# Kernel tuning notes

Hardware: AMD Instinct MI355X
Metric: run time of the kernel (lower is better)

Reference implementation:

```python
import jax, jax.numpy as jnp
import numpy as np

D_MODEL = 768
N_HEAD = 12
D_HEAD = 64


def setup_inputs() -> dict:
    key = jax.random.key(0)
    k1, k2, k3, k4, k5 = jax.random.split(key, 5)
    B, T = 8, 1024
    hidden_states = jax.random.normal(k1, (B, T, D_MODEL), dtype=jnp.float32)
    # torch Linear weights are [out, in]; we store [in, out] and use x @ W
    scale_attn = 1.0 / np.sqrt(D_MODEL)
    W_attn = jax.random.normal(k2, (D_MODEL, 3 * D_MODEL), dtype=jnp.float32) * scale_attn
    b_attn = jax.random.normal(k3, (3 * D_MODEL,), dtype=jnp.float32) * 0.02
    W_proj = jax.random.normal(k4, (D_MODEL, D_MODEL), dtype=jnp.float32) * scale_attn
    b_proj = jax.random.normal(k5, (D_MODEL,), dtype=jnp.float32) * 0.02
    return {"hidden_states": hidden_states, "W_attn": W_attn, "b_attn": b_attn,
            "W_proj": W_proj, "b_proj": b_proj}


def reference(hidden_states, W_attn, b_attn, W_proj, b_proj):
    B, T, _ = hidden_states.shape
    qkv = hidden_states @ W_attn + b_attn                     # [B, T, 3*D]
    Q, K, V = jnp.split(qkv, 3, axis=-1)
    def heads(x):  # [B, T, D] -> [B, H, T, d]
        return x.reshape(B, T, N_HEAD, D_HEAD).transpose(0, 2, 1, 3)
    Q, K, V = heads(Q), heads(K), heads(V)
    # past_key_values=None -> T_full == T, q_start == 0: standard causal mask
    scores = jnp.einsum('bhqd,bhkd->bhqk', Q, K) / np.sqrt(D_HEAD)
    causal = jnp.tril(jnp.ones((T, T), dtype=bool))
    scores = jnp.where(causal, scores, -jnp.inf)
    attn = jax.nn.softmax(scores, axis=-1)
    values = jnp.einsum('bhqk,bhkd->bhqd', attn, V)          # dropout = identity (eval)
    values = values.transpose(0, 2, 1, 3).reshape(B, T, D_MODEL)
    out = values @ W_proj + b_proj
    return out, K, V
```

## Files before the change

### kernel.cpp

```cpp
#include <hip/hip_runtime.h>
#include <stdint.h>

#define B_SZ 8
#define T_SZ 1024
#define DM   768
#define NH   12
#define DH   64
#define NTOK (B_SZ * T_SZ)
#define NOUT (NTOK * DM)
#define INF  __builtin_inff()

typedef unsigned short u16;
typedef __attribute__((ext_vector_type(8))) short short8;
typedef __attribute__((ext_vector_type(4))) short short4v;
typedef __attribute__((ext_vector_type(4))) float f32x4;

#define MFMA16x16x32 __builtin_amdgcn_mfma_f32_16x16x32_bf16

__device__ __forceinline__ u16 f2bf(float f) {
    unsigned u = __builtin_bit_cast(unsigned, f);
    u += 0x7fffu + ((u >> 16) & 1u);
    return (u16)(u >> 16);
}

__device__ __forceinline__ f32x4 max4(f32x4 a, f32x4 b) {
    f32x4 r; r.x = fmaxf(a.x, b.x); r.y = fmaxf(a.y, b.y);
    r.z = fmaxf(a.z, b.z); r.w = fmaxf(a.w, b.w); return r;
}
__device__ __forceinline__ f32x4 add4(f32x4 a, f32x4 b) {
    f32x4 r; r.x = a.x + b.x; r.y = a.y + b.y;
    r.z = a.z + b.z; r.w = a.w + b.w; return r;
}

__device__ __forceinline__ void gload16(const void* g, void* l) {
    __builtin_amdgcn_global_load_lds(
        (const __attribute__((address_space(1))) unsigned int*)(unsigned long long)(uintptr_t)g,
        (__attribute__((address_space(3))) unsigned int*)(unsigned int)(uintptr_t)l,
        16, 0, 0);
}

__global__ __launch_bounds__(256) void prep_kernel(
    const float* __restrict__ hs, u16* __restrict__ Xbf,
    const float* __restrict__ Wa, u16* __restrict__ WaT,
    const float* __restrict__ Wp, u16* __restrict__ WpT)
{
    __shared__ float tile[32][33];
    const int bid = blockIdx.x;
    if (bid < 6144) {
        const int i = bid * 1024 + threadIdx.x * 4;
        f32x4 v = *(const f32x4*)(hs + i);
        short4v o;
        o.x = (short)f2bf(v.x); o.y = (short)f2bf(v.y);
        o.z = (short)f2bf(v.z); o.w = (short)f2bf(v.w);
        *(short4v*)(Xbf + i) = o;
        return;
    }
    const float* in; u16* out; int R, C, bx, by;
    if (bid < 6144 + 1728) {
        const int lid = bid - 6144;
        in = Wa; out = WaT; R = 768; C = 2304; bx = lid % 72; by = lid / 72;
    } else {
        const int lid = bid - 7872;
        in = Wp; out = WpT; R = 768; C = 768; bx = lid % 24; by = lid / 24;
    }
    const int tx = threadIdx.x & 31, ty = threadIdx.x >> 5;
    const int c0 = bx * 32, r0 = by * 32;
    for (int i = ty; i < 32; i += 8)
        tile[i][tx] = in[(size_t)(r0 + i) * C + c0 + tx];
    __syncthreads();
    for (int i = ty; i < 32; i += 8)
        out[(size_t)(c0 + i) * R + r0 + tx] = f2bf(tile[tx][i]);
}

template <int EPI>
__global__ __launch_bounds__(256, 3) void gemm_k768_kernel(
    const u16* __restrict__ A, const u16* __restrict__ BT, const float* __restrict__ bias,
    u16* __restrict__ qbf, u16* __restrict__ kbf, u16* __restrict__ vtb,
    float* __restrict__ outK, float* __restrict__ outV, float* __restrict__ outP)
{
    __shared__ alignas(16) u16 SMEM[24576];
#define ASP(b) (SMEM + (b) * 4096)
#define BSP(b) (SMEM + 12288 + (b) * 4096)
    const int t   = threadIdx.x;
    const int wid = t >> 6, l = t & 63;
    const int lr  = l & 15, g = l >> 4;
    const int m0  = blockIdx.x * 128, n0 = blockIdx.y * 128;
    const int wm  = (wid >> 1) * 64, wn = (wid & 1) * 64;

    const int srow = t >> 2;
    const int sch  = ((t & 3) ^ ((srow >> 1) & 3)) * 8;
    const u16* ga0 = A  + (size_t)(m0 + srow) * 768 + sch;
    const u16* ga1 = A  + (size_t)(m0 + 64 + srow) * 768 + sch;
    const u16* gb0 = BT + (size_t)(n0 + srow) * 768 + sch;
    const u16* gb1 = BT + (size_t)(n0 + 64 + srow) * 768 + sch;

#define GSTAGE(buf, kt) do {                              \
        gload16(ga0 + (kt) * 32, ASP(buf) + t * 8);       \
        gload16(ga1 + (kt) * 32, ASP(buf) + 2048 + t * 8);\
        gload16(gb0 + (kt) * 32, BSP(buf) + t * 8);       \
        gload16(gb1 + (kt) * 32, BSP(buf) + 2048 + t * 8);\
    } while (0)

    const int fco = (g ^ ((lr >> 1) & 3)) * 8;

    f32x4 acc[4][4] = {};

#define COMPUTE(buf) do {                                                 \
        const u16* aB = ASP(buf);                                         \
        const u16* bB = BSP(buf);                                         \
        short8 af[4], bfr[4];                                             \
        _Pragma("unroll")                                                 \
        for (int i = 0; i < 4; ++i)                                       \
            af[i] = *(const short8*)(aB + (wm + i * 16 + lr) * 32 + fco); \
        _Pragma("unroll")                                                 \
        for (int j = 0; j < 4; ++j)                                       \
            bfr[j] = *(const short8*)(bB + (wn + j * 16 + lr) * 32 + fco);\
        __builtin_amdgcn_s_setprio(1);                                    \
        _Pragma("unroll")                                                 \
        for (int i = 0; i < 4; ++i)                                       \
            _Pragma("unroll")                                             \
            for (int j = 0; j < 4; ++j)                                   \
                acc[i][j] = MFMA16x16x32(af[i], bfr[j], acc[i][j], 0, 0, 0);\
        __builtin_amdgcn_s_setprio(0);                                    \
    } while (0)

#define WAITBAR(N) do {                                           \
        asm volatile("s_waitcnt vmcnt(" #N ")" ::: "memory");     \
        __builtin_amdgcn_s_barrier();                             \
        __builtin_amdgcn_sched_barrier(0);                        \
    } while (0)

    GSTAGE(0, 0); GSTAGE(1, 1);
    WAITBAR(4);

    #pragma unroll 1
    for (int i = 0; i < 7; ++i) {
        const int kt = i * 3;
        GSTAGE(2, kt + 2); COMPUTE(0); WAITBAR(4);
        GSTAGE(0, kt + 3); COMPUTE(1); WAITBAR(4);
        GSTAGE(1, kt + 4); COMPUTE(2); WAITBAR(4);
    }
    GSTAGE(2, 23); COMPUTE(0); WAITBAR(4);
    COMPUTE(1); WAITBAR(0);
    COMPUTE(2);
#undef GSTAGE
#undef COMPUTE
#undef WAITBAR

    if (EPI == 0) {
        __builtin_amdgcn_s_barrier();
        u16* EL = SMEM + wid * 4608;
        const int nbase = n0 + wn;
        const int which = nbase / 768;
        const int h = ((nbase - which * 768) >> 6);
        const int b = (m0 + wm) >> 10, tt0 = (m0 + wm) & 1023;
        const size_t rowbase = (size_t)(b * 12 + h) * 1024 + tt0;
        if (which == 0) {
            #pragma unroll
            for (int j = 0; j < 4; ++j) {
                const float bn = bias[nbase + j * 16 + lr];
                #pragma unroll
                for (int i = 0; i < 4; ++i)
                    #pragma unroll
                    for (int r = 0; r < 4; ++r) {
                        const int tau = i * 16 + g * 4 + r;
                        EL[tau * 72 + j * 16 + lr] =
                            f2bf((acc[i][j][r] + bn) * (0.125f * 1.44269504f));
                    }
            }
            asm volatile("s_waitcnt lgkmcnt(0)" ::: "memory");
            __builtin_amdgcn_sched_barrier(0);
            #pragma unroll
            for (int it = 0; it < 8; ++it) {
                const int q = it * 64 + l;
                const int tau = q >> 3, c = q & 7;
                *(short8*)(qbf + (rowbase + tau) * 64 + c * 8) =
                    *(const short8*)(EL + tau * 72 + c * 8);
            }
        } else if (which == 1) {
            #pragma unroll
            for (int j = 0; j < 4; ++j) {
                const float bn = bias[nbase + j * 16 + lr];
                #pragma unroll
                for (int i = 0; i < 4; ++i)
                    #pragma unroll
                    for (int r = 0; r < 4; ++r) {
                        const int tau = i * 16 + g * 4 + r;
                        const float v = acc[i][j][r] + bn;
                        EL[tau * 72 + j * 16 + lr] = f2bf(v);
                        outK[(rowbase + tau) * 64 + j * 16 + lr] = v;
                    }
            }
            asm volatile("s_waitcnt lgkmcnt(0)" ::: "memory");
            __builtin_amdgcn_sched_barrier(0);
            #pragma unroll
            for (int it = 0; it < 8; ++it) {
                const int q = it * 64 + l;
                const int tau = q >> 3, c = q & 7;
                *(short8*)(kbf + (rowbase + tau) * 64 + c * 8) =
                    *(const short8*)(EL + tau * 72 + c * 8);
            }
        } else {
            #pragma unroll
            for (int j = 0; j < 4; ++j) {
                const float bn = bias[nbase + j * 16 + lr];
                #pragma unroll
                for (int i = 0; i < 4; ++i)
                    #pragma unroll
                    for (int r = 0; r < 4; ++r) {
                        const int tau = i * 16 + g * 4 + r;
                        const float v = acc[i][j][r] + bn;
                        outV[(rowbase + tau) * 64 + j * 16 + lr] = v;
                        EL[(j * 16 + lr) * 72 + tau] = f2bf(v);
                    }
            }
            asm volatile("s_waitcnt lgkmcnt(0)" ::: "memory");
            __builtin_amdgcn_sched_barrier(0);
            u16* vt = vtb + (size_t)(b * 12 + h) * 65536 + tt0;
            #pragma unroll
            for (int it = 0; it < 8; ++it) {
                const int q = it * 64 + l;
                const int dd = q >> 3, c = q & 7;
                *(short8*)(vt + (size_t)dd * 1024 + c * 8) =
                    *(const short8*)(EL + dd * 72 + c * 8);
            }
        }
    } else {
        #pragma unroll
        for (int j = 0; j < 4; ++j) {
            const int n = n0 + wn + j * 16 + lr;
            const float bn = bias[n];
            #pragma unroll
            for (int i = 0; i < 4; ++i)
                #pragma unroll
                for (int r = 0; r < 4; ++r) {
                    const int m = m0 + wm + i * 16 + g * 4 + r;
                    outP[(size_t)m * 768 + n] = acc[i][j][r] + bn;
                }
        }
    }
#undef ASP
#undef BSP
}

__global__ __launch_bounds__(256, 4) void gemm_proj_kernel(
    const u16* __restrict__ A, const u16* __restrict__ BT,
    const float* __restrict__ bias, float* __restrict__ outP)
{
    __shared__ alignas(16) u16 As[3][64 * 32];
    __shared__ alignas(16) u16 Bs[3][128 * 32];
    const int t   = threadIdx.x;
    const int wid = t >> 6, l = t & 63;
    const int lr  = l & 15, g = l >> 4;
    const int m0  = blockIdx.x * 64, n0 = blockIdx.y * 128;
    const int wm  = (wid >> 1) * 32, wn = (wid & 1) * 64;

    const int srow = t >> 2;
    const int sch  = ((t & 3) ^ ((srow >> 1) & 3)) * 8;
    const u16* ga0 = A  + (size_t)(m0 + srow) * 768 + sch;
    const u16* gb0 = BT + (size_t)(n0 + srow) * 768 + sch;
    const u16* gb1 = BT + (size_t)(n0 + 64 + srow) * 768 + sch;

#define GSTAGE(buf, kt) do {                              \
        gload16(ga0 + (kt) * 32, As[buf] + t * 8);        \
        gload16(gb0 + (kt) * 32, Bs[buf] + t * 8);        \
        gload16(gb1 + (kt) * 32, Bs[buf] + 2048 + t * 8); \
    } while (0)

    const int fco = (g ^ ((lr >> 1) & 3)) * 8;

    f32x4 acc[2][4] = {};

#define COMPUTE(buf) do {                                                 \
        const u16* aB = As[buf];                                          \
        const u16* bB = Bs[buf];                                          \
        short8 af[2], bfr[4];                                             \
        _Pragma("unroll")                                                 \
        for (int i = 0; i < 2; ++i)                                       \
            af[i] = *(const short8*)(aB + (wm + i * 16 + lr) * 32 + fco); \
        _Pragma("unroll")                                                 \
        for (int j = 0; j < 4; ++j)                                       \
            bfr[j] = *(const short8*)(bB + (wn + j * 16 + lr) * 32 + fco);\
        __builtin_amdgcn_s_setprio(1);                                    \
        _Pragma("unroll")                                                 \
        for (int i = 0; i < 2; ++i)                                       \
            _Pragma("unroll")                                             \
            for (int j = 0; j < 4; ++j)                                   \
                acc[i][j] = MFMA16x16x32(af[i], bfr[j], acc[i][j], 0, 0, 0);\
        __builtin_amdgcn_s_setprio(0);                                    \
    } while (0)

#define WAITBAR(N) do {                                           \
        asm volatile("s_waitcnt vmcnt(" #N ")" ::: "memory");     \
        __builtin_amdgcn_s_barrier();                             \
        __builtin_amdgcn_sched_barrier(0);                        \
    } while (0)

    GSTAGE(0, 0); GSTAGE(1, 1);
    WAITBAR(3);

    #pragma unroll 1
    for (int i = 0; i < 7; ++i) {
        const int kt = i * 3;
        GSTAGE(2, kt + 2); COMPUTE(0); WAITBAR(3);
        GSTAGE(0, kt + 3); COMPUTE(1); WAITBAR(3);
        GSTAGE(1, kt + 4); COMPUTE(2); WAITBAR(3);
    }
    GSTAGE(2, 23); COMPUTE(0); WAITBAR(3);
    COMPUTE(1); WAITBAR(0);
    COMPUTE(2);
#undef GSTAGE
#undef COMPUTE
#undef WAITBAR

    #pragma unroll
    for (int j = 0; j < 4; ++j) {
        const int n = n0 + wn + j * 16 + lr;
        const float bn = bias[n];
        #pragma unroll
        for (int i = 0; i < 2; ++i)
            #pragma unroll
            for (int r = 0; r < 4; ++r) {
                const int m = m0 + wm + i * 16 + g * 4 + r;
                outP[(size_t)m * 768 + n] = acc[i][j][r] + bn;
            }
    }
}

__global__ __launch_bounds__(256, 4) void attn_kernel(
    const u16* __restrict__ Qb, const u16* __restrict__ Kb,
    const u16* __restrict__ Vt, u16* __restrict__ Ob)
{
    __shared__ alignas(16) u16 Ks[2][4096];
    __shared__ alignas(16) u16 Vs[4096];
    __shared__ alignas(16) u16 Pl[4][16 * 72];
    const int bh = blockIdx.x;
    const int t = threadIdx.x;
    const int wid = t >> 6, l = t & 63;
    const int c = l & 15, g = l >> 4;
    u16* P = Pl[wid];
    const u16* Kp = Kb + (size_t)bh * 65536;
    const u16* Vp = Vt + (size_t)bh * 65536;
    const int b = bh / 12, h = bh - (bh / 12) * 12;

    const int srow = t >> 3;
    const int sch  = (t & 7) ^ (srow & 7);
    const u16* Ksrc0 = Kp + (size_t)srow * 64 + sch * 8;
    const u16* Ksrc1 = Kp + (size_t)(srow + 32) * 64 + sch * 8;
    const u16* Vsrc0 = Vp + (size_t)srow * 1024 + sch * 8;
    const u16* Vsrc1 = Vp + (size_t)(srow + 32) * 1024 + sch * 8;

    const int fo0 = c * 64 + ((g ^ (c & 7)) * 8);
    const int fo1 = c * 64 + (((g + 4) ^ (c & 7)) * 8);

#define STAGE_K(buf, kt0) do {                                      \
        gload16(Ksrc0 + (size_t)(kt0) * 64, Ks[buf] + t * 8);       \
        gload16(Ksrc1 + (size_t)(kt0) * 64, Ks[buf] + 2048 + t * 8);\
    } while (0)
#define STAGE_V(kt0) do {                                           \
        gload16(Vsrc0 + (kt0), Vs + t * 8);                         \
        gload16(Vsrc1 + (kt0), Vs + 2048 + t * 8);                  \
    } while (0)

    #pragma unroll 1
    for (int pass = 0; pass < 2; ++pass) {
        const int tile = pass ? (15 - blockIdx.y) : blockIdx.y;
        const int qbase = tile * 64 + wid * 16;
        const int qg = qbase + c;
        const u16* Qp = Qb + ((size_t)bh * 1024 + qg) * 64 + g * 8;
        const short8 bq0 = *(const short8*)(Qp);
        const short8 bq1 = *(const short8*)(Qp + 32);

        f32x4 oacc[4] = {};
        float mrow = -INF, lpart = 0.f;
        const int nb = tile + 1;

        STAGE_K(0, 0);
        __syncthreads();
        int cur = 0;

        #pragma unroll 1
        for (int kb = 0; kb < nb; ++kb) {
            const int kt0 = kb << 6;
            STAGE_V(kt0);
            if (kb + 1 < nb) STAGE_K(cur ^ 1, kt0 + 64);
            const u16* kB = Ks[cur];
            short8 af0[4], af1[4];
            #pragma unroll
            for (int j = 0; j < 4; ++j) {
                af0[j] = *(const short8*)(kB + j * 1024 + fo0);
                af1[j] = *(const short8*)(kB + j * 1024 + fo1);
            }
            f32x4 s[4] = {};
            __builtin_amdgcn_s_setprio(1);
            #pragma unroll
            for (int j = 0; j < 4; ++j) {
                s[j] = MFMA16x16x32(af0[j], bq0, s[j], 0, 0, 0);
                s[j] = MFMA16x16x32(af1[j], bq1, s[j], 0, 0, 0);
            }
            __builtin_amdgcn_s_setprio(0);
            if (kb == nb - 1) {
                #pragma unroll
                for (int j = 0; j < 4; ++j)
                    #pragma unroll
                    for (int r = 0; r < 4; ++r)
                        if (kt0 + j * 16 + g * 4 + r > qg) s[j][r] = -INF;
            }
            f32x4 mm = max4(max4(s[0], s[1]), max4(s[2], s[3]));
            float tm = fmaxf(fmaxf(mm.x, mm.y), fmaxf(mm.z, mm.w));
            tm = fmaxf(tm, __shfl_xor(tm, 16));
            tm = fmaxf(tm, __shfl_xor(tm, 32));
            const bool keep = (__all(tm <= mrow + 8.f) != 0);
            const float mnew = keep ? mrow : fmaxf(mrow, tm);
            if (!keep) {
                const float sc = exp2f(mrow - mnew);
                mrow = mnew;
                lpart *= sc;
                #pragma unroll
                for (int dt = 0; dt < 4; ++dt) {
                    oacc[dt][0] *= sc; oacc[dt][1] *= sc;
                    oacc[dt][2] *= sc; oacc[dt][3] *= sc;
                }
            }
            f32x4 p[4];
            #pragma unroll
            for (int j = 0; j < 4; ++j) {
                p[j].x = exp2f(s[j].x - mnew); p[j].y = exp2f(s[j].y - mnew);
                p[j].z = exp2f(s[j].z - mnew); p[j].w = exp2f(s[j].w - mnew);
            }
            f32x4 ps = add4(add4(p[0], p[1]), add4(p[2], p[3]));
            lpart += (ps.x + ps.y) + (ps.z + ps.w);
            #pragma unroll
            for (int j = 0; j < 4; ++j) {
                short4v w;
                w.x = (short)f2bf(p[j].x); w.y = (short)f2bf(p[j].y);
                w.z = (short)f2bf(p[j].z); w.w = (short)f2bf(p[j].w);
                *(short4v*)(P + c * 72 + j * 16 + g * 4) = w;
            }
            asm volatile("s_waitcnt vmcnt(0)" ::: "memory");
            __builtin_amdgcn_s_barrier();
            __builtin_amdgcn_sched_barrier(0);
            const short8 pf0 = *(const short8*)(P + c * 72 + g * 8);
            const short8 pf1 = *(const short8*)(P + c * 72 + 32 + g * 8);
            short8 vf0[4], vf1[4];
            #pragma unroll
            for (int dt = 0; dt < 4; ++dt) {
                vf0[dt] = *(const short8*)(Vs + dt * 1024 + fo0);
                vf1[dt] = *(const short8*)(Vs + dt * 1024 + fo1);
            }
            __builtin_amdgcn_s_setprio(1);
            #pragma unroll
            for (int dt = 0; dt < 4; ++dt) {
                oacc[dt] = MFMA16x16x32(vf0[dt], pf0, oacc[dt], 0, 0, 0);
                oacc[dt] = MFMA16x16x32(vf1[dt], pf1, oacc[dt], 0, 0, 0);
            }
            __builtin_amdgcn_s_setprio(0);
            __syncthreads();
            cur ^= 1;
        }
        float lsum = lpart;
        lsum += __shfl_xor(lsum, 16);
        lsum += __shfl_xor(lsum, 32);
        const float li = 1.f / lsum;
        #pragma unroll
        for (int dt = 0; dt < 4; ++dt) {
            short4v o;
            o.x = (short)f2bf(oacc[dt][0] * li);
            o.y = (short)f2bf(oacc[dt][1] * li);
            o.z = (short)f2bf(oacc[dt][2] * li);
            o.w = (short)f2bf(oacc[dt][3] * li);
            *(short4v*)(Ob + (size_t)(b * 1024 + qg) * 768 + h * 64 + dt * 16 + g * 4) = o;
        }
    }
#undef STAGE_K
#undef STAGE_V
}

extern "C" void kernel_launch(void* const* d_in, const int* in_sizes, int n_in,
                              void* d_out, int out_size, void* d_ws, size_t ws_size,
                              hipStream_t stream) {
    const float* hs = (const float*)d_in[0];
    const float* Wa = (const float*)d_in[1];
    const float* ba = (const float*)d_in[2];
    const float* Wp = (const float*)d_in[3];
    const float* bp = (const float*)d_in[4];
    float* out = (float*)d_out;

    u16* ws  = (u16*)d_ws;
    u16* Xbf = ws;
    u16* WaT = Xbf + NOUT;
    u16* WpT = WaT + 768 * 2304;
    u16* Qbf = WpT + 768 * 768;
    u16* Kbf = Qbf + NOUT;
    u16* VTb = Kbf + NOUT;
    u16* Obf = VTb + NOUT;

    prep_kernel<<<8448, 256, 0, stream>>>(hs, Xbf, Wa, WaT, Wp, WpT);
    gemm_k768_kernel<0><<<dim3(64, 18), 256, 0, stream>>>(
        Xbf, WaT, ba, Qbf, Kbf, VTb, out + NOUT, out + 2 * (size_t)NOUT, nullptr);
    attn_kernel<<<dim3(96, 8), 256, 0, stream>>>(Qbf, Kbf, VTb, Obf);
    gemm_proj_kernel<<<dim3(128, 6), 256, 0, stream>>>(Obf, WpT, bp, out);
}
```

Baseline: 112.9 us.

## Double-buffer V with K, drop mid-loop barrier, coalesce attention output stores

V tiles now get their own double buffer and are prefetched one block ahead together with K, in a single staging step. This lets the loop drop the explicit vmcnt wait and workgroup barrier that sat between the softmax and the PV MFMAs, and V fragments are read from LDS early. The output tile is first written into the per-wave P scratch and then stored as 16-byte row-contiguous chunks, so global writes are coalesced. The extra LDS for the second V buffer lowers launch bounds from 4 to 3 blocks per CU. Without any vmcnt wait, correctness depends on the end-of-loop __syncthreads also waiting for the asynchronous global-to-LDS loads.

```diff
diff --git a/kernel.cpp b/kernel.cpp
--- a/kernel.cpp
+++ b/kernel.cpp
@@ -327,12 +327,12 @@
     }
 }
 
-__global__ __launch_bounds__(256, 4) void attn_kernel(
+__global__ __launch_bounds__(256, 3) void attn_kernel(
     const u16* __restrict__ Qb, const u16* __restrict__ Kb,
     const u16* __restrict__ Vt, u16* __restrict__ Ob)
 {
     __shared__ alignas(16) u16 Ks[2][4096];
-    __shared__ alignas(16) u16 Vs[4096];
+    __shared__ alignas(16) u16 Vs[2][4096];
     __shared__ alignas(16) u16 Pl[4][16 * 72];
     const int bh = blockIdx.x;
     const int t = threadIdx.x;
@@ -353,13 +353,11 @@
     const int fo0 = c * 64 + ((g ^ (c & 7)) * 8);
     const int fo1 = c * 64 + (((g + 4) ^ (c & 7)) * 8);
 
-#define STAGE_K(buf, kt0) do {                                      \
+#define STAGE(buf, kt0) do {                                        \
         gload16(Ksrc0 + (size_t)(kt0) * 64, Ks[buf] + t * 8);       \
         gload16(Ksrc1 + (size_t)(kt0) * 64, Ks[buf] + 2048 + t * 8);\
-    } while (0)
-#define STAGE_V(kt0) do {                                           \
-        gload16(Vsrc0 + (kt0), Vs + t * 8);                         \
-        gload16(Vsrc1 + (kt0), Vs + 2048 + t * 8);                  \
+        gload16(Vsrc0 + (kt0),              Vs[buf] + t * 8);       \
+        gload16(Vsrc1 + (kt0),              Vs[buf] + 2048 + t * 8);\
     } while (0)
 
     #pragma unroll 1
@@ -375,22 +373,26 @@
         float mrow = -INF, lpart = 0.f;
         const int nb = tile + 1;
 
-        STAGE_K(0, 0);
+        STAGE(0, 0);
         __syncthreads();
         int cur = 0;
 
         #pragma unroll 1
         for (int kb = 0; kb < nb; ++kb) {
-            const int kt0 = kb << 6;
-            STAGE_V(kt0);
-            if (kb + 1 < nb) STAGE_K(cur ^ 1, kt0 + 64);
+            if (kb + 1 < nb) STAGE(cur ^ 1, (kb + 1) << 6);
             const u16* kB = Ks[cur];
-            short8 af0[4], af1[4];
+            const u16* vB = Vs[cur];
+            short8 af0[4], af1[4], vf0[4], vf1[4];
             #pragma unroll
             for (int j = 0; j < 4; ++j) {
                 af0[j] = *(const short8*)(kB + j * 1024 + fo0);
                 af1[j] = *(const short8*)(kB + j * 1024 + fo1);
             }
+            #pragma unroll
+            for (int dt = 0; dt < 4; ++dt) {
+                vf0[dt] = *(const short8*)(vB + dt * 1024 + fo0);
+                vf1[dt] = *(const short8*)(vB + dt * 1024 + fo1);
+            }
             f32x4 s[4] = {};
             __builtin_amdgcn_s_setprio(1);
             #pragma unroll
@@ -400,6 +402,7 @@
             }
             __builtin_amdgcn_s_setprio(0);
             if (kb == nb - 1) {
+                const int kt0 = kb << 6;
                 #pragma unroll
                 for (int j = 0; j < 4; ++j)
                     #pragma unroll
@@ -437,17 +440,8 @@
                 w.z = (short)f2bf(p[j].z); w.w = (short)f2bf(p[j].w);
                 *(short4v*)(P + c * 72 + j * 16 + g * 4) = w;
             }
-            asm volatile("s_waitcnt vmcnt(0)" ::: "memory");
-            __builtin_amdgcn_s_barrier();
-            __builtin_amdgcn_sched_barrier(0);
             const short8 pf0 = *(const short8*)(P + c * 72 + g * 8);
             const short8 pf1 = *(const short8*)(P + c * 72 + 32 + g * 8);
-            short8 vf0[4], vf1[4];
-            #pragma unroll
-            for (int dt = 0; dt < 4; ++dt) {
-                vf0[dt] = *(const short8*)(Vs + dt * 1024 + fo0);
-                vf1[dt] = *(const short8*)(Vs + dt * 1024 + fo1);
-            }
             __builtin_amdgcn_s_setprio(1);
             #pragma unroll
             for (int dt = 0; dt < 4; ++dt) {
@@ -464,16 +458,24 @@
         const float li = 1.f / lsum;
         #pragma unroll
         for (int dt = 0; dt < 4; ++dt) {
-            short4v o;
-            o.x = (short)f2bf(oacc[dt][0] * li);
-            o.y = (short)f2bf(oacc[dt][1] * li);
-            o.z = (short)f2bf(oacc[dt][2] * li);
-            o.w = (short)f2bf(oacc[dt][3] * li);
-            *(short4v*)(Ob + (size_t)(b * 1024 + qg) * 768 + h * 64 + dt * 16 + g * 4) = o;
+            short4v w;
+            w.x = (short)f2bf(oacc[dt][0] * li);
+            w.y = (short)f2bf(oacc[dt][1] * li);
+            w.z = (short)f2bf(oacc[dt][2] * li);
+            w.w = (short)f2bf(oacc[dt][3] * li);
+            *(short4v*)(P + c * 72 + dt * 16 + g * 4) = w;
         }
-    }
-#undef STAGE_K
-#undef STAGE_V
+        asm volatile("s_waitcnt lgkmcnt(0)" ::: "memory");
+        __builtin_amdgcn_sched_barrier(0);
+        #pragma unroll
+        for (int it = 0; it < 2; ++it) {
+            const int idx = it * 64 + l;
+            const int q = idx >> 3, ch = idx & 7;
+            *(short8*)(Ob + (size_t)(b * 1024 + qbase + q) * 768 + h * 64 + ch * 8) =
+                *(const short8*)(P + q * 72 + ch * 8);
+        }
+    }
+#undef STAGE
 }
 
 extern "C" void kernel_launch(void* const* d_in, const int* in_sizes, int n_in,
```

Result: no change. 113.5 us (+0.6%).
